# Optimization experiments

Measured on AMD Instinct MI355X. Metric: run time of the kernel, lower is better.

Reference implementation:

```python
import jax, jax.numpy as jnp
import numpy as np

NUM_EMBEDDINGS = 1024
EMBEDDING_DIM = 64
COMMITMENT_COST = 0.25


def setup_inputs() -> dict:
    key = jax.random.key(0)
    k1, k2 = jax.random.split(key)
    z = jax.random.normal(k1, (32, EMBEDDING_DIM, 64, 64), dtype=jnp.float32)
    # nn.Embedding weight initialized uniform(-1/K, 1/K)
    lim = 1.0 / NUM_EMBEDDINGS
    codebook = jax.random.uniform(k2, (NUM_EMBEDDINGS, EMBEDDING_DIM),
                                  dtype=jnp.float32, minval=-lim, maxval=lim)
    return {"z": z, "codebook": codebook}


def reference(z, codebook):
    B, D, H, W = z.shape
    # (B, D, H, W) -> (B*H*W, D)
    z_flat = jnp.transpose(z, (0, 2, 3, 1)).reshape(-1, D)
    # squared L2 distances to all codebook entries: (N, K)
    distances = (jnp.sum(z_flat * z_flat, axis=1, keepdims=True)
                 + jnp.sum(codebook * codebook, axis=1)
                 - 2.0 * (z_flat @ codebook.T))
    encoding_indices = jnp.argmin(distances, axis=1)  # (N,)
    z_q = codebook[encoding_indices]                   # (N, D) gather
    z_q = jnp.transpose(z_q.reshape(B, H, W, D), (0, 3, 1, 2))
    vq_loss = jnp.mean((jax.lax.stop_gradient(z_q) - z) ** 2)
    commitment_loss = jnp.mean((z_q - jax.lax.stop_gradient(z)) ** 2)
    loss = vq_loss + COMMITMENT_COST * commitment_loss
    # straight-through estimator
    z_q_st = z + jax.lax.stop_gradient(z_q - z)
    return z_q_st, loss, encoding_indices.reshape(B, H * W)
```

## Files before the change

### kernel.cpp

```cpp
#include <hip/hip_runtime.h>

#define ZN 131072
#define DD 64
#define KK 1024
#define BSTRIDE 262144
#define DSTRIDE 4096
#define ZQ_ELEMS 8388608

#define WS_CSQ_OFF   16
#define WS_ZSQ_OFF   4112
#define WS_WORK_OFF  528400
#define WS_GMIN_OFF  1052688
#define WS_CBB_OFF   2363408

#define RF_CAND 16

typedef __attribute__((ext_vector_type(8))) short short8;
typedef __attribute__((ext_vector_type(4))) float f32x4;

__device__ __forceinline__ unsigned short f2bf_rne(float x) {
    unsigned u = __float_as_uint(x);
    return (unsigned short)((u + 0x7fffu + ((u >> 16) & 1u)) >> 16);
}

__device__ __forceinline__ float np_sumsq64(const float* a) {
    float r0 = __fmul_rn(a[0], a[0]), r1 = __fmul_rn(a[1], a[1]);
    float r2 = __fmul_rn(a[2], a[2]), r3 = __fmul_rn(a[3], a[3]);
    float r4 = __fmul_rn(a[4], a[4]), r5 = __fmul_rn(a[5], a[5]);
    float r6 = __fmul_rn(a[6], a[6]), r7 = __fmul_rn(a[7], a[7]);
#pragma unroll
    for (int i = 8; i < 64; i += 8) {
        r0 = __fadd_rn(r0, __fmul_rn(a[i + 0], a[i + 0]));
        r1 = __fadd_rn(r1, __fmul_rn(a[i + 1], a[i + 1]));
        r2 = __fadd_rn(r2, __fmul_rn(a[i + 2], a[i + 2]));
        r3 = __fadd_rn(r3, __fmul_rn(a[i + 3], a[i + 3]));
        r4 = __fadd_rn(r4, __fmul_rn(a[i + 4], a[i + 4]));
        r5 = __fadd_rn(r5, __fmul_rn(a[i + 5], a[i + 5]));
        r6 = __fadd_rn(r6, __fmul_rn(a[i + 6], a[i + 6]));
        r7 = __fadd_rn(r7, __fmul_rn(a[i + 7], a[i + 7]));
    }
    return __fadd_rn(__fadd_rn(__fadd_rn(r0, r1), __fadd_rn(r2, r3)),
                     __fadd_rn(__fadd_rn(r4, r5), __fadd_rn(r6, r7)));
}

__global__ __launch_bounds__(256) void vq_csq(const float* __restrict__ cb,
                                              float* __restrict__ csq) {
    int k = blockIdx.x * 256 + threadIdx.x;
    csq[k] = np_sumsq64(cb + k * DD);
}

__global__ __launch_bounds__(256) void vq_prep_b(const float* __restrict__ cb,
                                                 unsigned short* __restrict__ cbB) {
    int i = blockIdx.x * 256 + threadIdx.x;
    int k = i >> 6, d = i & 63;
    float c = cb[i];
    unsigned short hi = f2bf_rne(c);
    float hf = __uint_as_float((unsigned)hi << 16);
    unsigned short lo = f2bf_rne(c - hf);
    int ct = k >> 4, col = k & 15;
    int s = d >> 5, lg = (d >> 3) & 3, j = d & 7;
    int lane = col + 16 * lg;
    int base = ct * 2048 + s * 512 + lane * 8 + j;
    cbB[base] = hi;
    cbB[base + 1024] = lo;
}

__global__ __launch_bounds__(256) void vq_zsq(const float* __restrict__ z,
                                              float* __restrict__ zsq32) {
    int n = blockIdx.x * 256 + threadIdx.x;
    int b = n >> 12, p = n & 4095;
    const float* zp = z + (size_t)b * BSTRIDE + p;
    float r[8];
#pragma unroll
    for (int j = 0; j < 8; ++j) {
        float v = zp[(size_t)j * DSTRIDE];
        r[j] = __fmul_rn(v, v);
    }
#pragma unroll
    for (int i = 8; i < 64; i += 8)
#pragma unroll
        for (int j = 0; j < 8; ++j) {
            float v = zp[(size_t)(i + j) * DSTRIDE];
            r[j] = __fadd_rn(r[j], __fmul_rn(v, v));
        }
    zsq32[n] = __fadd_rn(__fadd_rn(__fadd_rn(r[0], r[1]), __fadd_rn(r[2], r[3])),
                         __fadd_rn(__fadd_rn(r[4], r[5]), __fadd_rn(r[6], r[7])));
}

#define MFMA_DIST(P, Q, A_H0, A_H1, A_L0, A_L1, B0, B1, B2, B3)               \
    P = __builtin_amdgcn_mfma_f32_16x16x32_bf16(A_H0, B0, P, 0, 0, 0);        \
    Q = __builtin_amdgcn_mfma_f32_16x16x32_bf16(A_H0, B2, Q, 0, 0, 0);        \
    P = __builtin_amdgcn_mfma_f32_16x16x32_bf16(A_H1, B1, P, 0, 0, 0);        \
    Q = __builtin_amdgcn_mfma_f32_16x16x32_bf16(A_H1, B3, Q, 0, 0, 0);        \
    P = __builtin_amdgcn_mfma_f32_16x16x32_bf16(A_L0, B0, P, 0, 0, 0);        \
    Q = __builtin_amdgcn_mfma_f32_16x16x32_bf16(A_L1, B1, Q, 0, 0, 0);

__global__ __launch_bounds__(256)
void vq_scan(const float* __restrict__ z,
             const unsigned short* __restrict__ cbB,
             const float* __restrict__ csq,
             float* __restrict__ idxf_out,
             float* __restrict__ gminbuf,
             unsigned* __restrict__ wcount,
             int* __restrict__ worklist) {
    __shared__ __align__(16) unsigned short aFrag[4][2][2][64][8];
    __shared__ float scsq[1024];
    __shared__ float rmin1[64], rmin2[64];
    __shared__ int rbest[64];

    int t = threadIdx.x;
    int n0 = blockIdx.x * 64;
    int b = n0 >> 12, p0 = n0 & 4095;

    for (int i = t; i < 1024; i += 256) scsq[i] = csq[i];

    {
        int r = t & 63, gb = t >> 6;
        const float* zp = z + (size_t)b * BSTRIDE + p0 + r;
#pragma unroll
        for (int gg = 0; gg < 2; ++gg) {
            int g = (gb << 1) | gg;
            short8 hi8, lo8;
#pragma unroll
            for (int i2 = 0; i2 < 8; ++i2) {
                float v = zp[(size_t)(8 * g + i2) * DSTRIDE];
                unsigned short h = f2bf_rne(v);
                float hf = __uint_as_float((unsigned)h << 16);
                hi8[i2] = (short)h;
                lo8[i2] = (short)f2bf_rne(v - hf);
            }
            int rt = r >> 4, s = g >> 2, lane = (r & 15) + 16 * (g & 3);
            *(short8*)&aFrag[rt][s][0][lane][0] = hi8;
            *(short8*)&aFrag[rt][s][1][lane][0] = lo8;
        }
    }
    __syncthreads();

    int l = t & 63;
    int colcode = l & 15;
    int w = __builtin_amdgcn_readfirstlane(t >> 6);

    short8 aH0 = *(const short8*)&aFrag[w][0][0][l][0];
    short8 aH1 = *(const short8*)&aFrag[w][1][0][l][0];
    short8 aL0 = *(const short8*)&aFrag[w][0][1][l][0];
    short8 aL1 = *(const short8*)&aFrag[w][1][1][l][0];

    float m1[4], m2[4];
    int bst[4];
#pragma unroll
    for (int r = 0; r < 4; ++r) {
        m1[r] = 3.4e38f;
        m2[r] = 3.4e38f;
        bst[r] = 0;
    }

    for (int ph = 0; ph < 8; ++ph) {
        __syncthreads();
#pragma unroll 2
        for (int c8 = 0; c8 < 8; ++c8) {
            int ct = ph * 8 + c8;
            const unsigned short* bp = cbB + ct * 2048 + (l << 3);
            short8 b0 = *(const short8*)(bp);
            short8 b1 = *(const short8*)(bp + 512);
            short8 b2 = *(const short8*)(bp + 1024);
            short8 b3 = *(const short8*)(bp + 1536);
            float cs = scsq[(ct << 4) + colcode];
            int code = (ct << 4) + colcode;
            f32x4 p = {0.f, 0.f, 0.f, 0.f}, q = {0.f, 0.f, 0.f, 0.f};
            MFMA_DIST(p, q, aH0, aH1, aL0, aL1, b0, b1, b2, b3)
#pragma unroll
            for (int r = 0; r < 4; ++r) {
                float dist = fmaf(-2.f, p[r] + q[r], cs);
                bool lt = dist < m1[r];
                m2[r] = lt ? m1[r] : fminf(m2[r], dist);
                bst[r] = lt ? code : bst[r];
                m1[r] = lt ? dist : m1[r];
            }
        }
    }

#pragma unroll
    for (int m = 1; m <= 8; m <<= 1) {
#pragma unroll
        for (int r = 0; r < 4; ++r) {
            float o1 = __shfl_xor(m1[r], m, 64);
            float o2 = __shfl_xor(m2[r], m, 64);
            int ob = __shfl_xor(bst[r], m, 64);
            bool take = (o1 < m1[r]) || (o1 == m1[r] && ob < bst[r]);
            float n2 = take ? fminf(o2, m1[r]) : fminf(m2[r], o1);
            m1[r] = take ? o1 : m1[r];
            bst[r] = take ? ob : bst[r];
            m2[r] = n2;
        }
    }

#pragma unroll
    for (int r = 0; r < 4; ++r)
        if (colcode == r) {
            int row = (w << 4) + ((l >> 4) << 2) + r;
            rmin1[row] = m1[r];
            rmin2[row] = m2[r];
            rbest[row] = bst[r];
        }
    __syncthreads();

    if (t < 64) {
        float g1 = rmin1[t], g2 = rmin2[t];
        int gb = rbest[t];
        int n = n0 + t;
        idxf_out[n] = (float)gb;
        gminbuf[n] = g1;
        bool flag = (g2 - g1 < 2e-4f);
        unsigned long long mb = __ballot(flag);
        int tot = __popcll(mb);
        unsigned base = 0;
        if (t == 0 && tot) base = atomicAdd(wcount, (unsigned)tot);
        base = __shfl(base, 0, 64);
        if (flag) {
            int pre = __popcll(mb & ((1ull << t) - 1ull));
            worklist[base + pre] = n;
        }
    }
}

__global__ __launch_bounds__(256)
void vq_refine(const float* __restrict__ z,
               const unsigned short* __restrict__ cbB,
               const float* __restrict__ cb,
               const float* __restrict__ csq,
               const float* __restrict__ zsq32,
               const float* __restrict__ gminbuf,
               const unsigned* __restrict__ wcount,
               const int* __restrict__ worklist,
               float* __restrict__ idxf) {
    __shared__ __align__(16) unsigned short aFrag[4][2][2][64][8];
    __shared__ float scsq[1024];
    __shared__ int rown[64];
    __shared__ float rgminS[64];
    __shared__ int candCnt[64];
    __shared__ unsigned short candK[64][RF_CAND];
    __shared__ unsigned long long rpack[64];

    int t = threadIdx.x;
    int l = t & 63;
    int colcode = l & 15;
    int w = __builtin_amdgcn_readfirstlane(t >> 6);

    for (int i = t; i < 1024; i += 256) scsq[i] = csq[i];

    unsigned cnt = *wcount;
    for (unsigned c0 = blockIdx.x * 64u; c0 < cnt; c0 += gridDim.x * 64u) {
        int nrows = (int)((cnt - c0 < 64u) ? (cnt - c0) : 64u);
        if (t < 64) {
            int n = worklist[(t < nrows) ? (c0 + t) : c0];
            rown[t] = n;
            rgminS[t] = gminbuf[n];
            candCnt[t] = 0;
            rpack[t] = ~0ull;
        }
        __syncthreads();

        {
            int r = t & 63, gb = t >> 6;
            int n = rown[r];
            int b = n >> 12, p = n & 4095;
            const float* zp = z + (size_t)b * BSTRIDE + p;
#pragma unroll
            for (int gg = 0; gg < 2; ++gg) {
                int g = (gb << 1) | gg;
                short8 hi8, lo8;
#pragma unroll
                for (int i2 = 0; i2 < 8; ++i2) {
                    float v = zp[(size_t)(8 * g + i2) * DSTRIDE];
                    unsigned short h = f2bf_rne(v);
                    float hf = __uint_as_float((unsigned)h << 16);
                    hi8[i2] = (short)h;
                    lo8[i2] = (short)f2bf_rne(v - hf);
                }
                int rt = r >> 4, s = g >> 2, lane = (r & 15) + 16 * (g & 3);
                *(short8*)&aFrag[rt][s][0][lane][0] = hi8;
                *(short8*)&aFrag[rt][s][1][lane][0] = lo8;
            }
        }
        __syncthreads();

        short8 aH0 = *(const short8*)&aFrag[w][0][0][l][0];
        short8 aH1 = *(const short8*)&aFrag[w][1][0][l][0];
        short8 aL0 = *(const short8*)&aFrag[w][0][1][l][0];
        short8 aL1 = *(const short8*)&aFrag[w][1][1][l][0];

        int rowbase = (w << 4) + ((l >> 4) << 2);
        float rg[4];
#pragma unroll
        for (int r = 0; r < 4; ++r) rg[r] = rgminS[rowbase + r] + 2e-4f;

        for (int ct = 0; ct < 64; ++ct) {
            const unsigned short* bp = cbB + ct * 2048 + (l << 3);
            short8 b0 = *(const short8*)(bp);
            short8 b1 = *(const short8*)(bp + 512);
            short8 b2 = *(const short8*)(bp + 1024);
            short8 b3 = *(const short8*)(bp + 1536);
            float cs = scsq[(ct << 4) + colcode];
            unsigned code = (unsigned)((ct << 4) + colcode);
            f32x4 p = {0.f, 0.f, 0.f, 0.f}, q = {0.f, 0.f, 0.f, 0.f};
            MFMA_DIST(p, q, aH0, aH1, aL0, aL1, b0, b1, b2, b3)
#pragma unroll
            for (int r = 0; r < 4; ++r) {
                float dist = fmaf(-2.f, p[r] + q[r], cs);
                if (dist < rg[r]) {
                    int row = rowbase + r;
                    int pos = atomicAdd(&candCnt[row], 1);
                    if (pos < RF_CAND) candK[row][pos] = (unsigned short)code;
                }
            }
        }
        __syncthreads();

        for (int i = t; i < 64 * RF_CAND; i += 256) {
            int r = i >> 4, sIdx = i & (RF_CAND - 1);
            int cc = candCnt[r];
            if (r < nrows && cc <= RF_CAND && sIdx < cc) {
                unsigned k = candK[r][sIdx];
                int n = rown[r];
                int b = n >> 12, p = n & 4095;
                const float* zp = z + (size_t)b * BSTRIDE + p;
                const float* cp = cb + k * DD;
                double a0 = 0.0, a1 = 0.0, a2 = 0.0, a3 = 0.0;
#pragma unroll
                for (int d = 0; d < DD; d += 4) {
                    a0 = fma((double)zp[(size_t)(d + 0) * DSTRIDE], (double)cp[d + 0], a0);
                    a1 = fma((double)zp[(size_t)(d + 1) * DSTRIDE], (double)cp[d + 1], a1);
                    a2 = fma((double)zp[(size_t)(d + 2) * DSTRIDE], (double)cp[d + 2], a2);
                    a3 = fma((double)zp[(size_t)(d + 3) * DSTRIDE], (double)cp[d + 3], a3);
                }
                double dot = (a0 + a1) + (a2 + a3);
                float twoC = (float)(2.0 * dot);
                float dist = __fsub_rn(__fadd_rn(zsq32[n], csq[k]), twoC);
                unsigned ub = __float_as_uint(dist);
                ub = (ub & 0x80000000u) ? ~ub : (ub | 0x80000000u);
                unsigned long long pk = ((unsigned long long)ub << 32) | k;
                atomicMin(&rpack[r], pk);
            }
        }
        for (int r = 0; r < 64; ++r) {
            if (candCnt[r] > RF_CAND && r < nrows) {
                int n = rown[r];
                int b = n >> 12, p = n & 4095;
                const float* zp = z + (size_t)b * BSTRIDE + p;
                for (unsigned k = (unsigned)t; k < 1024u; k += 256u) {
                    const float* cp = cb + k * DD;
                    double a0 = 0.0, a1 = 0.0, a2 = 0.0, a3 = 0.0;
#pragma unroll
                    for (int d = 0; d < DD; d += 4) {
                        a0 = fma((double)zp[(size_t)(d + 0) * DSTRIDE], (double)cp[d + 0], a0);
                        a1 = fma((double)zp[(size_t)(d + 1) * DSTRIDE], (double)cp[d + 1], a1);
                        a2 = fma((double)zp[(size_t)(d + 2) * DSTRIDE], (double)cp[d + 2], a2);
                        a3 = fma((double)zp[(size_t)(d + 3) * DSTRIDE], (double)cp[d + 3], a3);
                    }
                    double dot = (a0 + a1) + (a2 + a3);
                    float twoC = (float)(2.0 * dot);
                    float dist = __fsub_rn(__fadd_rn(zsq32[n], csq[k]), twoC);
                    unsigned ub = __float_as_uint(dist);
                    ub = (ub & 0x80000000u) ? ~ub : (ub | 0x80000000u);
                    unsigned long long pk = ((unsigned long long)ub << 32) | k;
                    atomicMin(&rpack[r], pk);
                }
            }
        }
        __syncthreads();

        if (t < nrows)
            idxf[rown[t]] = (float)(unsigned)(rpack[t] & 0xFFFFFFFFull);
        __syncthreads();
    }
}

__global__ __launch_bounds__(256) void vq_gather_loss(const float* __restrict__ z,
                                                      const float* __restrict__ cb,
                                                      const float* __restrict__ idxf,
                                                      float* __restrict__ zq_out,
                                                      double* __restrict__ acc) {
    int n = blockIdx.x * 256 + threadIdx.x;
    int b = n >> 12, p = n & 4095;
    const float* zp = z + (size_t)b * BSTRIDE + p;
    float* qp = zq_out + (size_t)b * BSTRIDE + p;
    int k = (int)idxf[n];
    const float* c = cb + k * DD;

    float s = 0.f;
#pragma unroll
    for (int d = 0; d < DD; ++d) {
        float q = c[d];
        float diff = q - zp[(size_t)d * DSTRIDE];
        s = fmaf(diff, diff, s);
        qp[(size_t)d * DSTRIDE] = q;
    }

#pragma unroll
    for (int off = 32; off; off >>= 1) s += __shfl_down(s, off, 64);
    __shared__ float partial[4];
    if ((threadIdx.x & 63) == 0) partial[threadIdx.x >> 6] = s;
    __syncthreads();
    if (threadIdx.x == 0) {
        float t = (partial[0] + partial[1]) + (partial[2] + partial[3]);
        atomicAdd(acc, (double)t);
    }
}

__global__ void vq_finalize(const double* __restrict__ acc, float* __restrict__ loss_out) {
    *loss_out = (float)(1.25 * (*acc) / (double)ZQ_ELEMS);
}

extern "C" void kernel_launch(void* const* d_in, const int* in_sizes, int n_in,
                              void* d_out, int out_size, void* d_ws, size_t ws_size,
                              hipStream_t stream) {
    const float* z = (const float*)d_in[0];
    const float* cb = (const float*)d_in[1];
    float* out = (float*)d_out;

    float* zq_out = out;
    float* loss_out = out + ZQ_ELEMS;
    float* idxf_out = out + ZQ_ELEMS + 1;

    char* ws = (char*)d_ws;
    double* acc = (double*)ws;
    unsigned* wcount = (unsigned*)(ws + 8);
    float* csq = (float*)(ws + WS_CSQ_OFF);
    float* zsq32 = (float*)(ws + WS_ZSQ_OFF);
    int* worklist = (int*)(ws + WS_WORK_OFF);
    float* gminbuf = (float*)(ws + WS_GMIN_OFF);
    unsigned short* cbB = (unsigned short*)(ws + WS_CBB_OFF);

    hipMemsetAsync(d_ws, 0, 16, stream);

    vq_csq<<<KK / 256, 256, 0, stream>>>(cb, csq);
    vq_prep_b<<<KK * DD / 256, 256, 0, stream>>>(cb, cbB);
    vq_zsq<<<ZN / 256, 256, 0, stream>>>(z, zsq32);
    vq_scan<<<ZN / 64, 256, 0, stream>>>(z, cbB, csq, idxf_out, gminbuf, wcount, worklist);
    vq_refine<<<768, 256, 0, stream>>>(z, cbB, cb, csq, zsq32, gminbuf, wcount, worklist, idxf_out);
    vq_gather_loss<<<ZN / 256, 256, 0, stream>>>(z, cb, idxf_out, zq_out, acc);
    vq_finalize<<<1, 1, 0, stream>>>(acc, loss_out);
}
```

Baseline: 257.5 us.

## Fuse refine pass into scan kernel and prefetch codebook fragments

```diff
diff --git a/kernel.cpp b/kernel.cpp
--- a/kernel.cpp
+++ b/kernel.cpp
@@ -9,8 +9,6 @@
 
 #define WS_CSQ_OFF   16
 #define WS_ZSQ_OFF   4112
-#define WS_WORK_OFF  528400
-#define WS_GMIN_OFF  1052688
 #define WS_CBB_OFF   2363408
 
 #define RF_CAND 16
@@ -95,24 +93,52 @@
     P = __builtin_amdgcn_mfma_f32_16x16x32_bf16(A_L0, B0, P, 0, 0, 0);        \
     Q = __builtin_amdgcn_mfma_f32_16x16x32_bf16(A_L1, B1, Q, 0, 0, 0);
 
-__global__ __launch_bounds__(256)
+__device__ __forceinline__ unsigned long long ref_pack(const float* zp,
+                                                       const float* cp,
+                                                       float zsqn, float csqk,
+                                                       unsigned k) {
+    double a0 = 0.0, a1 = 0.0, a2 = 0.0, a3 = 0.0;
+#pragma unroll
+    for (int d = 0; d < DD; d += 4) {
+        a0 = fma((double)zp[(size_t)(d + 0) * DSTRIDE], (double)cp[d + 0], a0);
+        a1 = fma((double)zp[(size_t)(d + 1) * DSTRIDE], (double)cp[d + 1], a1);
+        a2 = fma((double)zp[(size_t)(d + 2) * DSTRIDE], (double)cp[d + 2], a2);
+        a3 = fma((double)zp[(size_t)(d + 3) * DSTRIDE], (double)cp[d + 3], a3);
+    }
+    double dot = (a0 + a1) + (a2 + a3);
+    float twoC = (float)(2.0 * dot);
+    float dist = __fsub_rn(__fadd_rn(zsqn, csqk), twoC);
+    unsigned ub = __float_as_uint(dist);
+    ub = (ub & 0x80000000u) ? ~ub : (ub | 0x80000000u);
+    return ((unsigned long long)ub << 32) | k;
+}
+
+__global__ __attribute__((amdgpu_waves_per_eu(4, 4))) __launch_bounds__(256)
 void vq_scan(const float* __restrict__ z,
              const unsigned short* __restrict__ cbB,
+             const float* __restrict__ cb,
              const float* __restrict__ csq,
-             float* __restrict__ idxf_out,
-             float* __restrict__ gminbuf,
-             unsigned* __restrict__ wcount,
-             int* __restrict__ worklist) {
+             const float* __restrict__ zsq32,
+             float* __restrict__ idxf_out) {
     __shared__ __align__(16) unsigned short aFrag[4][2][2][64][8];
     __shared__ float scsq[1024];
     __shared__ float rmin1[64], rmin2[64];
     __shared__ int rbest[64];
+    __shared__ float rthr[64];
+    __shared__ unsigned rtmask[4];
+    __shared__ int candCnt[64];
+    __shared__ unsigned short candK[64][RF_CAND];
+    __shared__ unsigned long long rpack[64];
 
     int t = threadIdx.x;
     int n0 = blockIdx.x * 64;
     int b = n0 >> 12, p0 = n0 & 4095;
 
     for (int i = t; i < 1024; i += 256) scsq[i] = csq[i];
+    if (t < 64) {
+        candCnt[t] = 0;
+        rpack[t] = ~0ull;
+    }
 
     {
         int r = t & 63, gb = t >> 6;
@@ -154,16 +180,24 @@
         bst[r] = 0;
     }
 
+    const unsigned short* bpb = cbB + (l << 3);
+    short8 nb0 = *(const short8*)(bpb);
+    short8 nb1 = *(const short8*)(bpb + 512);
+    short8 nb2 = *(const short8*)(bpb + 1024);
+    short8 nb3 = *(const short8*)(bpb + 1536);
     for (int ph = 0; ph < 8; ++ph) {
         __syncthreads();
 #pragma unroll 2
         for (int c8 = 0; c8 < 8; ++c8) {
-            int ct = ph * 8 + c8;
-            const unsigned short* bp = cbB + ct * 2048 + (l << 3);
-            short8 b0 = *(const short8*)(bp);
-            short8 b1 = *(const short8*)(bp + 512);
-            short8 b2 = *(const short8*)(bp + 1024);
-            short8 b3 = *(const short8*)(bp + 1536);
+            int ct = (ph << 3) | c8;
+            short8 b0 = nb0, b1 = nb1, b2 = nb2, b3 = nb3;
+            if (ct < 63) {
+                const unsigned short* np = bpb + (ct + 1) * 2048;
+                nb0 = *(const short8*)(np);
+                nb1 = *(const short8*)(np + 512);
+                nb2 = *(const short8*)(np + 1024);
+                nb3 = *(const short8*)(np + 1536);
+            }
             float cs = scsq[(ct << 4) + colcode];
             int code = (ct << 4) + colcode;
             f32x4 p = {0.f, 0.f, 0.f, 0.f}, q = {0.f, 0.f, 0.f, 0.f};
@@ -205,96 +239,30 @@
     __syncthreads();
 
     if (t < 64) {
-        float g1 = rmin1[t], g2 = rmin2[t];
-        int gb = rbest[t];
-        int n = n0 + t;
-        idxf_out[n] = (float)gb;
-        gminbuf[n] = g1;
-        bool flag = (g2 - g1 < 2e-4f);
+        bool flag = (rmin2[t] - rmin1[t] < 2e-4f);
+        rthr[t] = flag ? rmin1[t] + 2e-4f : -3.4e38f;
         unsigned long long mb = __ballot(flag);
-        int tot = __popcll(mb);
-        unsigned base = 0;
-        if (t == 0 && tot) base = atomicAdd(wcount, (unsigned)tot);
-        base = __shfl(base, 0, 64);
-        if (flag) {
-            int pre = __popcll(mb & ((1ull << t) - 1ull));
-            worklist[base + pre] = n;
-        }
-    }
-}
-
-__global__ __launch_bounds__(256)
-void vq_refine(const float* __restrict__ z,
-               const unsigned short* __restrict__ cbB,
-               const float* __restrict__ cb,
-               const float* __restrict__ csq,
-               const float* __restrict__ zsq32,
-               const float* __restrict__ gminbuf,
-               const unsigned* __restrict__ wcount,
-               const int* __restrict__ worklist,
-               float* __restrict__ idxf) {
-    __shared__ __align__(16) unsigned short aFrag[4][2][2][64][8];
-    __shared__ float scsq[1024];
-    __shared__ int rown[64];
-    __shared__ float rgminS[64];
-    __shared__ int candCnt[64];
-    __shared__ unsigned short candK[64][RF_CAND];
-    __shared__ unsigned long long rpack[64];
-
-    int t = threadIdx.x;
-    int l = t & 63;
-    int colcode = l & 15;
-    int w = __builtin_amdgcn_readfirstlane(t >> 6);
-
-    for (int i = t; i < 1024; i += 256) scsq[i] = csq[i];
-
-    unsigned cnt = *wcount;
-    for (unsigned c0 = blockIdx.x * 64u; c0 < cnt; c0 += gridDim.x * 64u) {
-        int nrows = (int)((cnt - c0 < 64u) ? (cnt - c0) : 64u);
-        if (t < 64) {
-            int n = worklist[(t < nrows) ? (c0 + t) : c0];
-            rown[t] = n;
-            rgminS[t] = gminbuf[n];
-            candCnt[t] = 0;
-            rpack[t] = ~0ull;
-        }
-        __syncthreads();
-
-        {
-            int r = t & 63, gb = t >> 6;
-            int n = rown[r];
-            int b = n >> 12, p = n & 4095;
-            const float* zp = z + (size_t)b * BSTRIDE + p;
-#pragma unroll
-            for (int gg = 0; gg < 2; ++gg) {
-                int g = (gb << 1) | gg;
-                short8 hi8, lo8;
-#pragma unroll
-                for (int i2 = 0; i2 < 8; ++i2) {
-                    float v = zp[(size_t)(8 * g + i2) * DSTRIDE];
-                    unsigned short h = f2bf_rne(v);
-                    float hf = __uint_as_float((unsigned)h << 16);
-                    hi8[i2] = (short)h;
-                    lo8[i2] = (short)f2bf_rne(v - hf);
-                }
-                int rt = r >> 4, s = g >> 2, lane = (r & 15) + 16 * (g & 3);
-                *(short8*)&aFrag[rt][s][0][lane][0] = hi8;
-                *(short8*)&aFrag[rt][s][1][lane][0] = lo8;
-            }
-        }
-        __syncthreads();
-
-        short8 aH0 = *(const short8*)&aFrag[w][0][0][l][0];
-        short8 aH1 = *(const short8*)&aFrag[w][1][0][l][0];
-        short8 aL0 = *(const short8*)&aFrag[w][0][1][l][0];
-        short8 aL1 = *(const short8*)&aFrag[w][1][1][l][0];
-
-        int rowbase = (w << 4) + ((l >> 4) << 2);
-        float rg[4];
-#pragma unroll
-        for (int r = 0; r < 4; ++r) rg[r] = rgminS[rowbase + r] + 2e-4f;
-
-        for (int ct = 0; ct < 64; ++ct) {
+        if (t == 0) {
+            rtmask[0] = (unsigned)(mb & 0xFFFFull);
+            rtmask[1] = (unsigned)((mb >> 16) & 0xFFFFull);
+            rtmask[2] = (unsigned)((mb >> 32) & 0xFFFFull);
+            rtmask[3] = (unsigned)((mb >> 48) & 0xFFFFull);
+        }
+    }
+    __syncthreads();
+
+    for (int rt = 0; rt < 4; ++rt) {
+        unsigned fm = __builtin_amdgcn_readfirstlane(rtmask[rt]);
+        if (fm == 0) continue;
+        short8 cH0 = *(const short8*)&aFrag[rt][0][0][l][0];
+        short8 cH1 = *(const short8*)&aFrag[rt][1][0][l][0];
+        short8 cL0 = *(const short8*)&aFrag[rt][0][1][l][0];
+        short8 cL1 = *(const short8*)&aFrag[rt][1][1][l][0];
+        int rowb = (rt << 4) + ((l >> 4) << 2);
+        float th0 = rthr[rowb + 0], th1 = rthr[rowb + 1];
+        float th2 = rthr[rowb + 2], th3 = rthr[rowb + 3];
+        for (int ci = 0; ci < 16; ++ci) {
+            int ct = (w << 4) + ci;
             const unsigned short* bp = cbB + ct * 2048 + (l << 3);
             short8 b0 = *(const short8*)(bp);
             short8 b1 = *(const short8*)(bp + 512);
@@ -303,75 +271,58 @@
             float cs = scsq[(ct << 4) + colcode];
             unsigned code = (unsigned)((ct << 4) + colcode);
             f32x4 p = {0.f, 0.f, 0.f, 0.f}, q = {0.f, 0.f, 0.f, 0.f};
-            MFMA_DIST(p, q, aH0, aH1, aL0, aL1, b0, b1, b2, b3)
-#pragma unroll
-            for (int r = 0; r < 4; ++r) {
-                float dist = fmaf(-2.f, p[r] + q[r], cs);
-                if (dist < rg[r]) {
-                    int row = rowbase + r;
-                    int pos = atomicAdd(&candCnt[row], 1);
-                    if (pos < RF_CAND) candK[row][pos] = (unsigned short)code;
-                }
-            }
-        }
-        __syncthreads();
-
-        for (int i = t; i < 64 * RF_CAND; i += 256) {
-            int r = i >> 4, sIdx = i & (RF_CAND - 1);
-            int cc = candCnt[r];
-            if (r < nrows && cc <= RF_CAND && sIdx < cc) {
-                unsigned k = candK[r][sIdx];
-                int n = rown[r];
-                int b = n >> 12, p = n & 4095;
-                const float* zp = z + (size_t)b * BSTRIDE + p;
-                const float* cp = cb + k * DD;
-                double a0 = 0.0, a1 = 0.0, a2 = 0.0, a3 = 0.0;
-#pragma unroll
-                for (int d = 0; d < DD; d += 4) {
-                    a0 = fma((double)zp[(size_t)(d + 0) * DSTRIDE], (double)cp[d + 0], a0);
-                    a1 = fma((double)zp[(size_t)(d + 1) * DSTRIDE], (double)cp[d + 1], a1);
-                    a2 = fma((double)zp[(size_t)(d + 2) * DSTRIDE], (double)cp[d + 2], a2);
-                    a3 = fma((double)zp[(size_t)(d + 3) * DSTRIDE], (double)cp[d + 3], a3);
-                }
-                double dot = (a0 + a1) + (a2 + a3);
-                float twoC = (float)(2.0 * dot);
-                float dist = __fsub_rn(__fadd_rn(zsq32[n], csq[k]), twoC);
-                unsigned ub = __float_as_uint(dist);
-                ub = (ub & 0x80000000u) ? ~ub : (ub | 0x80000000u);
-                unsigned long long pk = ((unsigned long long)ub << 32) | k;
+            MFMA_DIST(p, q, cH0, cH1, cL0, cL1, b0, b1, b2, b3)
+            float d0 = fmaf(-2.f, p[0] + q[0], cs);
+            float d1 = fmaf(-2.f, p[1] + q[1], cs);
+            float d2 = fmaf(-2.f, p[2] + q[2], cs);
+            float d3 = fmaf(-2.f, p[3] + q[3], cs);
+            if (d0 < th0) {
+                int pos = atomicAdd(&candCnt[rowb + 0], 1);
+                if (pos < RF_CAND) candK[rowb + 0][pos] = (unsigned short)code;
+            }
+            if (d1 < th1) {
+                int pos = atomicAdd(&candCnt[rowb + 1], 1);
+                if (pos < RF_CAND) candK[rowb + 1][pos] = (unsigned short)code;
+            }
+            if (d2 < th2) {
+                int pos = atomicAdd(&candCnt[rowb + 2], 1);
+                if (pos < RF_CAND) candK[rowb + 2][pos] = (unsigned short)code;
+            }
+            if (d3 < th3) {
+                int pos = atomicAdd(&candCnt[rowb + 3], 1);
+                if (pos < RF_CAND) candK[rowb + 3][pos] = (unsigned short)code;
+            }
+        }
+    }
+    __syncthreads();
+
+    for (int i = t; i < 64 * RF_CAND; i += 256) {
+        int r = i >> 4, sIdx = i & (RF_CAND - 1);
+        int cc = candCnt[r];
+        if (cc > 0 && cc <= RF_CAND && sIdx < cc) {
+            unsigned k = candK[r][sIdx];
+            int n = n0 + r;
+            const float* zp = z + (size_t)b * BSTRIDE + p0 + r;
+            unsigned long long pk = ref_pack(zp, cb + k * DD, zsq32[n], csq[k], k);
+            atomicMin(&rpack[r], pk);
+        }
+    }
+    for (int r = 0; r < 64; ++r) {
+        if (candCnt[r] > RF_CAND) {
+            int n = n0 + r;
+            const float* zp = z + (size_t)b * BSTRIDE + p0 + r;
+            for (unsigned k = (unsigned)t; k < 1024u; k += 256u) {
+                unsigned long long pk = ref_pack(zp, cb + k * DD, zsq32[n], csq[k], k);
                 atomicMin(&rpack[r], pk);
             }
         }
-        for (int r = 0; r < 64; ++r) {
-            if (candCnt[r] > RF_CAND && r < nrows) {
-                int n = rown[r];
-                int b = n >> 12, p = n & 4095;
-                const float* zp = z + (size_t)b * BSTRIDE + p;
-                for (unsigned k = (unsigned)t; k < 1024u; k += 256u) {
-                    const float* cp = cb + k * DD;
-                    double a0 = 0.0, a1 = 0.0, a2 = 0.0, a3 = 0.0;
-#pragma unroll
-                    for (int d = 0; d < DD; d += 4) {
-                        a0 = fma((double)zp[(size_t)(d + 0) * DSTRIDE], (double)cp[d + 0], a0);
-                        a1 = fma((double)zp[(size_t)(d + 1) * DSTRIDE], (double)cp[d + 1], a1);
-                        a2 = fma((double)zp[(size_t)(d + 2) * DSTRIDE], (double)cp[d + 2], a2);
-                        a3 = fma((double)zp[(size_t)(d + 3) * DSTRIDE], (double)cp[d + 3], a3);
-                    }
-                    double dot = (a0 + a1) + (a2 + a3);
-                    float twoC = (float)(2.0 * dot);
-                    float dist = __fsub_rn(__fadd_rn(zsq32[n], csq[k]), twoC);
-                    unsigned ub = __float_as_uint(dist);
-                    ub = (ub & 0x80000000u) ? ~ub : (ub | 0x80000000u);
-                    unsigned long long pk = ((unsigned long long)ub << 32) | k;
-                    atomicMin(&rpack[r], pk);
-                }
-            }
-        }
-        __syncthreads();
-
-        if (t < nrows)
-            idxf[rown[t]] = (float)(unsigned)(rpack[t] & 0xFFFFFFFFull);
-        __syncthreads();
+    }
+    __syncthreads();
+
+    if (t < 64) {
+        unsigned long long pk = rpack[t];
+        int kk = (pk != ~0ull) ? (int)(unsigned)(pk & 0xFFFFFFFFull) : rbest[t];
+        idxf_out[n0 + t] = (float)kk;
     }
 }
 
@@ -424,11 +375,8 @@
 
     char* ws = (char*)d_ws;
     double* acc = (double*)ws;
-    unsigned* wcount = (unsigned*)(ws + 8);
     float* csq = (float*)(ws + WS_CSQ_OFF);
     float* zsq32 = (float*)(ws + WS_ZSQ_OFF);
-    int* worklist = (int*)(ws + WS_WORK_OFF);
-    float* gminbuf = (float*)(ws + WS_GMIN_OFF);
     unsigned short* cbB = (unsigned short*)(ws + WS_CBB_OFF);
 
     hipMemsetAsync(d_ws, 0, 16, stream);
@@ -436,8 +384,7 @@
     vq_csq<<<KK / 256, 256, 0, stream>>>(cb, csq);
     vq_prep_b<<<KK * DD / 256, 256, 0, stream>>>(cb, cbB);
     vq_zsq<<<ZN / 256, 256, 0, stream>>>(z, zsq32);
-    vq_scan<<<ZN / 64, 256, 0, stream>>>(z, cbB, csq, idxf_out, gminbuf, wcount, worklist);
-    vq_refine<<<768, 256, 0, stream>>>(z, cbB, cb, csq, zsq32, gminbuf, wcount, worklist, idxf_out);
+    vq_scan<<<ZN / 64, 256, 0, stream>>>(z, cbB, cb, csq, zsq32, idxf_out);
     vq_gather_loss<<<ZN / 256, 256, 0, stream>>>(z, cb, idxf_out, zq_out, acc);
     vq_finalize<<<1, 1, 0, stream>>>(acc, loss_out);
 }
```

Result: no change. 258.4 us (+0.4%).
